# Optimization experiments

Hardware: AMD Instinct MI355X
Metric: run time of the kernel (lower is better)

## Reference

```python
import jax, jax.numpy as jnp
import numpy as np

B, L, C, H = 32, 512, 512, 8
DH = C // H
LN_EPS = 1e-5


def setup_inputs() -> dict:
    key = jax.random.key(0)
    ks = jax.random.split(key, 5)
    x = jax.random.normal(ks[0], (B, L, C), dtype=jnp.float32)
    # nn.Linear weights are (out, in); y = x @ W.T
    wq = jax.random.normal(ks[1], (C, C), dtype=jnp.float32) * 0.02
    wk = jax.random.normal(ks[2], (C, C), dtype=jnp.float32) * 0.02
    wv = jax.random.normal(ks[3], (C, C), dtype=jnp.float32) * 0.02
    # source zero-inits the bias table; use small randoms so it actually contributes
    bias_table = jax.random.normal(ks[4], (2 * L - 1, H), dtype=jnp.float32) * 0.02
    gamma = jnp.ones((C,), dtype=jnp.float32)
    beta = jnp.zeros((C,), dtype=jnp.float32)
    coords = np.arange(L)
    rel_index = jnp.asarray(coords[None, :] - coords[:, None] + (L - 1), dtype=jnp.int32)  # (L, L)
    return {"x": x, "wq": wq, "wk": wk, "wv": wv, "bias_table": bias_table,
            "gamma": gamma, "beta": beta, "rel_index": rel_index}


def reference(x, wq, wk, wv, bias_table, gamma, beta, rel_index):
    Bx, Lx, Cx = x.shape
    scale = Cx ** (-0.5)  # note: scale uses full emb_size, as in source
    q = (x @ wq.T).reshape(Bx, Lx, H, DH).transpose(0, 2, 1, 3)  # (B,H,L,Dh)
    k = (x @ wk.T).reshape(Bx, Lx, H, DH).transpose(0, 2, 1, 3)
    v = (x @ wv.T).reshape(Bx, Lx, H, DH).transpose(0, 2, 1, 3)
    attn = jax.nn.softmax(jnp.einsum('bhqd,bhkd->bhqk', q, k) * scale, axis=-1)
    # post-softmax relative bias gather-add
    rel_bias = bias_table[rel_index]                # (L, L, H)
    attn = attn + rel_bias.transpose(2, 0, 1)[None]  # (1,H,L,L) broadcast
    out = jnp.einsum('bhqk,bhkd->bhqd', attn, v)
    out = out.transpose(0, 2, 1, 3).reshape(Bx, Lx, Cx)
    mu = out.mean(axis=-1, keepdims=True)
    var = jnp.mean(jnp.square(out - mu), axis=-1, keepdims=True)
    return gamma * (out - mu) * jax.lax.rsqrt(var + LN_EPS) + beta
```

## Files before the change

kernel.cpp:

```cpp
#include <hip/hip_runtime.h>
#include <hip/hip_bf16.h>

typedef unsigned short u16;
typedef __attribute__((ext_vector_type(8))) __bf16 bf16x8;
typedef __attribute__((ext_vector_type(4))) float f32x4;
typedef __attribute__((ext_vector_type(4))) unsigned int u32x4;

#define BB 32
#define LL 512
#define CC 512
#define HH 8
#define DH 64
#define MROWS (BB * LL)
#define NQKV  (3 * CC)

#define XB_BYTES ((size_t)MROWS * CC * 2)
#define WC_BYTES ((size_t)NQKV * CC * 2)
#define QKV_OFF  (XB_BYTES + WC_BYTES)

#define SCALE2 (0.044194173824159216f * 1.4426950408889634f)

__device__ inline u16 f2b(float f) {
  union { float f; unsigned u; } a; a.f = f;
  unsigned u = a.u;
  return (u16)((u + 0x7FFFu + ((u >> 16) & 1u)) >> 16);
}

__device__ inline unsigned pack2(float a, float b) {
  float2 f; f.x = a; f.y = b;
  union { __hip_bfloat162 h; unsigned u; } c;
  c.h = __float22bfloat162_rn(f);
  return c.u;
}

__device__ inline bf16x8 gload16(const u16* p) {
  u32x4 r;
  asm volatile("global_load_dwordx4 %0, %1, off" : "=v"(r) : "v"(p));
  return __builtin_bit_cast(bf16x8, r);
}

__global__ __launch_bounds__(256) void cvt_x(const float* __restrict__ x, u16* __restrict__ xb) {
  int i = blockIdx.x * 256 + threadIdx.x;
  float4 v = ((const float4*)x)[i];
  uint2 o; o.x = pack2(v.x, v.y); o.y = pack2(v.z, v.w);
  ((uint2*)xb)[i] = o;
}

__global__ __launch_bounds__(256) void cvt_w(const float* __restrict__ wq, const float* __restrict__ wk,
                                             const float* __restrict__ wv, u16* __restrict__ wcat) {
  int i = blockIdx.x * 256 + threadIdx.x;
  int e = i * 4;
  int n = e >> 9;
  int k = e & 511;
  const float* src = (n < 512) ? (wq + (size_t)n * 512)
                   : (n < 1024) ? (wk + (size_t)(n - 512) * 512)
                                : (wv + (size_t)(n - 1024) * 512);
  const float sc = (n < 512) ? SCALE2 : 1.0f;
  float4 v = *(const float4*)(src + k);
  uint2 o; o.x = pack2(v.x * sc, v.y * sc); o.y = pack2(v.z * sc, v.w * sc);
  *(uint2*)(wcat + (size_t)n * 512 + k) = o;
}

__global__ __launch_bounds__(256) void bias_trans(const float* __restrict__ bias_table,
                                                  float* __restrict__ biasT) {
  int i = blockIdx.x * 256 + threadIdx.x;
  if (i < 1023 * 8) {
    float v = bias_table[i];
    int rel = i >> 3, hh = i & 7;
    biasT[hh * 1024 + rel] = v;
  }
}

typedef __attribute__((address_space(1))) void* as1_void_p;
typedef __attribute__((address_space(3))) void* as3_void_p;

__device__ inline void async16(const u16* g, u16* l) {
#if __has_builtin(__builtin_amdgcn_global_load_lds)
  __builtin_amdgcn_global_load_lds((as1_void_p)g, (as3_void_p)l, 16, 0, 0);
#else
  *(uint4*)l = *(const uint4*)g;
#endif
}

__global__ __launch_bounds__(256) void gemm_qkv(const u16* __restrict__ A, const u16* __restrict__ Bw,
                                                u16* __restrict__ Cm) {
  __shared__ u16 a_lds[128 * 32];
  __shared__ u16 b_lds[128 * 32];
  const int n0 = blockIdx.x * 128, m0 = blockIdx.y * 128;
  const int t = threadIdx.x, l = t & 63;
  const int wrow = ((t >> 7) & 1) * 64, wcol = ((t >> 6) & 1) * 64;
  const int lr = l & 15, lq = l >> 4;

  f32x4 acc[4][4] = {};

  for (int k0 = 0; k0 < 512; k0 += 32) {
    {
      int c0 = t, c1 = t + 256;
      async16(A  + (size_t)(m0 + (c0 >> 2)) * 512 + k0 + (c0 & 3) * 8, &a_lds[c0 * 8]);
      async16(A  + (size_t)(m0 + (c1 >> 2)) * 512 + k0 + (c1 & 3) * 8, &a_lds[c1 * 8]);
      async16(Bw + (size_t)(n0 + (c0 >> 2)) * 512 + k0 + (c0 & 3) * 8, &b_lds[c0 * 8]);
      async16(Bw + (size_t)(n0 + (c1 >> 2)) * 512 + k0 + (c1 & 3) * 8, &b_lds[c1 * 8]);
    }
    __syncthreads();
    bf16x8 af[4], bfr[4];
#pragma unroll
    for (int r = 0; r < 4; ++r) af[r]  = *(const bf16x8*)&a_lds[(wrow + r * 16 + lr) * 32 + lq * 8];
#pragma unroll
    for (int c = 0; c < 4; ++c) bfr[c] = *(const bf16x8*)&b_lds[(wcol + c * 16 + lr) * 32 + lq * 8];
#pragma unroll
    for (int r = 0; r < 4; ++r)
#pragma unroll
      for (int c = 0; c < 4; ++c)
        acc[r][c] = __builtin_amdgcn_mfma_f32_16x16x32_bf16(af[r], bfr[c], acc[r][c], 0, 0, 0);
    __syncthreads();
  }
#pragma unroll
  for (int r = 0; r < 4; ++r) {
#pragma unroll
    for (int i = 0; i < 4; ++i) {
      int m = m0 + wrow + r * 16 + lq * 4 + i;
      u16* crow = Cm + (size_t)m * NQKV + n0 + wcol;
#pragma unroll
      for (int c = 0; c < 4; ++c)
        crow[c * 16 + lr] = f2b(acc[r][c][i]);
    }
  }
}

__global__ __launch_bounds__(256) void transpose_v(const u16* __restrict__ qkv, u16* __restrict__ vT) {
  const int bh = blockIdx.x;
  const int b = bh >> 3, h = bh & 7;
  const int lc0 = blockIdx.y * 128;
  __shared__ u16 tile[32 * 72];
  const int t = threadIdx.x;
  for (int lc = lc0; lc < lc0 + 128; lc += 32) {
    int lrow = t >> 3, dcol = (t & 7) * 8;
    const u16* src = qkv + (size_t)(b * 512 + lc + lrow) * NQKV + 1024 + h * 64 + dcol;
    *(uint4*)&tile[lrow * 72 + dcol] = *(const uint4*)src;
    __syncthreads();
    int d = t >> 2, lp = (t & 3) * 8;
    union { ushort4 v4[2]; u16 s[8]; } tmp;
#pragma unroll
    for (int j = 0; j < 8; ++j) tmp.s[j] = tile[(lp + j) * 72 + d];
    *(uint4*)&vT[(size_t)(bh * 64 + d) * 512 + lc + lp] = *(uint4*)&tmp;
    __syncthreads();
  }
}

__global__ __launch_bounds__(256, 4) void attn_kernel(const u16* __restrict__ qkv, const u16* __restrict__ vT,
                                                      const float* __restrict__ biasT,
                                                      float* __restrict__ out) {
  __shared__ u16 p_lds[32 * 512];
  __shared__ float bias_lds[544];
  __shared__ float reds[4][32];

  const int flat = blockIdx.x;
  const int bh = ((flat >> 7) << 3) | (flat & 7);
  const int q0 = ((flat >> 3) & 15) * 32;
  const int b = bh >> 3, h = bh & 7;
  const int t = threadIdx.x, l = t & 63, w = t >> 6;
  const int lr = l & 15, lq = l >> 4;

  {
    const int rel0 = 480 - q0;
    const float* bsrc = biasT + h * 1024 + rel0;
    for (int i = t; i < 543; i += 256)
      bias_lds[i] = bsrc[i];
  }

  bf16x8 bq[2][2];
#pragma unroll
  for (int qt = 0; qt < 2; ++qt) {
    const u16* qrow = qkv + (size_t)(b * 512 + q0 + qt * 16 + lr) * NQKV + h * 64;
    bq[qt][0] = *(const bf16x8*)(qrow + lq * 8);
    bq[qt][1] = *(const bf16x8*)(qrow + 32 + lq * 8);
  }

  const u16* kbase = qkv + (size_t)(b * 512 + w * 128 + lr) * NQKV + 512 + h * 64 + lq * 8;
  bf16x8 ak[8][2];
#pragma unroll
  for (int ct = 0; ct < 8; ++ct) {
    const u16* kr = kbase + (size_t)ct * 16 * NQKV;
    ak[ct][0] = gload16(kr);
    ak[ct][1] = gload16(kr + 32);
  }
  asm volatile("s_waitcnt vmcnt(0)" ::: "memory");
  __builtin_amdgcn_sched_barrier(0);

  f32x4 sT[2][8];
#pragma unroll
  for (int ct = 0; ct < 8; ++ct) {
    f32x4 a0 = {0.f, 0.f, 0.f, 0.f}, a1 = {0.f, 0.f, 0.f, 0.f};
    a0 = __builtin_amdgcn_mfma_f32_16x16x32_bf16(ak[ct][0], bq[0][0], a0, 0, 0, 0);
    a0 = __builtin_amdgcn_mfma_f32_16x16x32_bf16(ak[ct][1], bq[0][1], a0, 0, 0, 0);
    a1 = __builtin_amdgcn_mfma_f32_16x16x32_bf16(ak[ct][0], bq[1][0], a1, 0, 0, 0);
    a1 = __builtin_amdgcn_mfma_f32_16x16x32_bf16(ak[ct][1], bq[1][1], a1, 0, 0, 0);
    sT[0][ct] = a0;
    sT[1][ct] = a1;
  }

  float sloc[2];
#pragma unroll
  for (int qt = 0; qt < 2; ++qt) {
    float s0 = 0.f, s1 = 0.f, s2 = 0.f, s3 = 0.f;
#pragma unroll
    for (int ct = 0; ct < 8; ++ct) {
      float e0 = exp2f(sT[qt][ct][0]);
      float e1 = exp2f(sT[qt][ct][1]);
      float e2 = exp2f(sT[qt][ct][2]);
      float e3 = exp2f(sT[qt][ct][3]);
      sT[qt][ct][0] = e0; sT[qt][ct][1] = e1;
      sT[qt][ct][2] = e2; sT[qt][ct][3] = e3;
      s0 += e0; s1 += e1; s2 += e2; s3 += e3;
    }
    float s = (s0 + s1) + (s2 + s3);
    s += __shfl_xor(s, 16, 64);
    s += __shfl_xor(s, 32, 64);
    sloc[qt] = s;
  }
  if (lq == 0) { reds[w][lr] = sloc[0]; reds[w][16 + lr] = sloc[1]; }
  __syncthreads();
  float rinv[2];
#pragma unroll
  for (int qt = 0; qt < 2; ++qt)
    rinv[qt] = 1.0f / (reds[0][qt * 16 + lr] + reds[1][qt * 16 + lr] +
                       reds[2][qt * 16 + lr] + reds[3][qt * 16 + lr]);

  const u16* vrow = vT + (size_t)(bh * 64 + w * 16 + lr) * 512 + lq * 8;
  bf16x8 av[16];
#pragma unroll
  for (int kb = 0; kb < 8; ++kb) av[kb] = gload16(vrow + kb * 32);

#define PACK_QT(qt)                                                            \
  {                                                                            \
    const int qlocal = (qt) * 16 + lr;                                         \
    u16* prow = p_lds + qlocal * 512;                                          \
    const int boff = w * 128 + lq * 4 + 31 - qlocal;                           \
    _Pragma("unroll")                                                          \
    for (int ct = 0; ct < 8; ++ct) {                                           \
      const int gsw = w * 8 + (ct ^ (lr & 7));                                 \
      float p0 = sT[qt][ct][0] * rinv[qt] + bias_lds[boff + ct * 16 + 0];      \
      float p1 = sT[qt][ct][1] * rinv[qt] + bias_lds[boff + ct * 16 + 1];      \
      float p2 = sT[qt][ct][2] * rinv[qt] + bias_lds[boff + ct * 16 + 2];      \
      float p3 = sT[qt][ct][3] * rinv[qt] + bias_lds[boff + ct * 16 + 3];      \
      uint2 pk; pk.x = pack2(p0, p1); pk.y = pack2(p2, p3);                    \
      *(uint2*)&prow[gsw * 16 + lq * 4] = pk;                                  \
    }                                                                          \
  }

  PACK_QT(0)
#pragma unroll
  for (int kb = 8; kb < 16; ++kb) av[kb] = gload16(vrow + kb * 32);
  PACK_QT(1)
#undef PACK_QT

  __syncthreads();
  asm volatile("s_waitcnt vmcnt(0)" ::: "memory");
  __builtin_amdgcn_sched_barrier(0);

  f32x4 accP[2] = {};
  bf16x8 bp[4][2];
#define LDP(kb, qt) \
  (*(const bf16x8*)&p_lds[((qt) * 16 + lr) * 512 + \
    (((2 * (kb) + (lq >> 1)) & ~7) | (((2 * (kb) + (lq >> 1)) & 7) ^ (lr & 7))) * 16 + (lq & 1) * 8])
#pragma unroll
  for (int pre = 0; pre < 3; ++pre) { bp[pre][0] = LDP(pre, 0); bp[pre][1] = LDP(pre, 1); }
#pragma unroll
  for (int kb = 0; kb < 16; ++kb) {
    if (kb < 13) {
      bp[(kb + 3) & 3][0] = LDP(kb + 3, 0);
      bp[(kb + 3) & 3][1] = LDP(kb + 3, 1);
    }
    accP[0] = __builtin_amdgcn_mfma_f32_16x16x32_bf16(av[kb], bp[kb & 3][0], accP[0], 0, 0, 0);
    accP[1] = __builtin_amdgcn_mfma_f32_16x16x32_bf16(av[kb], bp[kb & 3][1], accP[1], 0, 0, 0);
  }
#undef LDP
#pragma unroll
  for (int qt = 0; qt < 2; ++qt)
    *(f32x4*)&out[(size_t)(b * 512 + q0 + qt * 16 + lr) * 512 + h * 64 + w * 16 + lq * 4] = accP[qt];
}

__global__ __launch_bounds__(256) void ln_kernel(float* __restrict__ out,
                                                 const float* __restrict__ gamma,
                                                 const float* __restrict__ beta) {
  const int t = threadIdx.x;
  const int r2 = t >> 7;
  const int row = blockIdx.x * 2 + r2;
  const int c = (t & 127) * 4;
  float* p = out + (size_t)row * 512;
  float4 v = *(float4*)(p + c);
  float s = v.x + v.y + v.z + v.w;
  float s2 = v.x * v.x + v.y * v.y + v.z * v.z + v.w * v.w;
#pragma unroll
  for (int d = 1; d < 64; d <<= 1) { s += __shfl_xor(s, d, 64); s2 += __shfl_xor(s2, d, 64); }
  __shared__ float ps[4], ps2[4];
  const int wv = t >> 6;
  if ((t & 63) == 0) { ps[wv] = s; ps2[wv] = s2; }
  __syncthreads();
  s  = ps[r2 * 2]  + ps[r2 * 2 + 1];
  s2 = ps2[r2 * 2] + ps2[r2 * 2 + 1];
  float mu = s * (1.0f / 512.0f);
  float var = s2 * (1.0f / 512.0f) - mu * mu;
  float rs = rsqrtf(var + 1e-5f);
  float4 g = *(const float4*)(gamma + c);
  float4 bb = *(const float4*)(beta + c);
  v.x = g.x * (v.x - mu) * rs + bb.x;
  v.y = g.y * (v.y - mu) * rs + bb.y;
  v.z = g.z * (v.z - mu) * rs + bb.z;
  v.w = g.w * (v.w - mu) * rs + bb.w;
  *(float4*)(p + c) = v;
}

extern "C" void kernel_launch(void* const* d_in, const int* in_sizes, int n_in,
                              void* d_out, int out_size, void* d_ws, size_t ws_size,
                              hipStream_t stream) {
  const float* x    = (const float*)d_in[0];
  const float* wq   = (const float*)d_in[1];
  const float* wk   = (const float*)d_in[2];
  const float* wv   = (const float*)d_in[3];
  const float* bias = (const float*)d_in[4];
  const float* gamma = (const float*)d_in[5];
  const float* beta  = (const float*)d_in[6];
  float* out = (float*)d_out;

  char* ws = (char*)d_ws;
  u16* xb   = (u16*)ws;
  u16* wcat = (u16*)(ws + XB_BYTES);
  u16* qkv  = (u16*)(ws + QKV_OFF);
  u16* vT   = xb;
  float* biasT = (float*)(ws + XB_BYTES);

  cvt_x<<<dim3((MROWS * CC) / 4 / 256), 256, 0, stream>>>(x, xb);
  cvt_w<<<dim3((NQKV * CC) / 4 / 256), 256, 0, stream>>>(wq, wk, wv, wcat);
  gemm_qkv<<<dim3(NQKV / 128, MROWS / 128), 256, 0, stream>>>(xb, wcat, qkv);
  bias_trans<<<dim3(32), 256, 0, stream>>>(bias, biasT);
  transpose_v<<<dim3(256, 4), 256, 0, stream>>>(qkv, vT);
  attn_kernel<<<dim3(16 * 256), 256, 0, stream>>>(qkv, vT, biasT, out);
  ln_kernel<<<dim3(MROWS / 2), 256, 0, stream>>>(out, gamma, beta);
}
```

Before: 227.8 us.

## Fold bias transpose into transpose_v, pair global loads, add MFMA priority hints

The separate bias_trans launch is merged into transpose_v as an extra grid row, which removes one kernel launch. In attn_kernel, K and V global loads are issued in pairs through inline asm using immediate offsets, which saves address arithmetic. The MFMA sections are wrapped in s_setprio raise and lower hints, and the occupancy hint in launch_bounds drops from 4 to 3 blocks per CU. The lower occupancy hint gives the compiler more registers but may reduce latency hiding.

```diff
diff --git a/kernel.cpp b/kernel.cpp
--- a/kernel.cpp
+++ b/kernel.cpp
@@ -31,12 +31,6 @@
   union { __hip_bfloat162 h; unsigned u; } c;
   c.h = __float22bfloat162_rn(f);
   return c.u;
-}
-
-__device__ inline bf16x8 gload16(const u16* p) {
-  u32x4 r;
-  asm volatile("global_load_dwordx4 %0, %1, off" : "=v"(r) : "v"(p));
-  return __builtin_bit_cast(bf16x8, r);
 }
 
 __global__ __launch_bounds__(256) void cvt_x(const float* __restrict__ x, u16* __restrict__ xb) {
@@ -61,16 +55,6 @@
   *(uint2*)(wcat + (size_t)n * 512 + k) = o;
 }
 
-__global__ __launch_bounds__(256) void bias_trans(const float* __restrict__ bias_table,
-                                                  float* __restrict__ biasT) {
-  int i = blockIdx.x * 256 + threadIdx.x;
-  if (i < 1023 * 8) {
-    float v = bias_table[i];
-    int rel = i >> 3, hh = i & 7;
-    biasT[hh * 1024 + rel] = v;
-  }
-}
-
 typedef __attribute__((address_space(1))) void* as1_void_p;
 typedef __attribute__((address_space(3))) void* as3_void_p;
 
@@ -127,7 +111,20 @@
   }
 }
 
-__global__ __launch_bounds__(256) void transpose_v(const u16* __restrict__ qkv, u16* __restrict__ vT) {
+__global__ __launch_bounds__(256) void transpose_v(const u16* __restrict__ qkv, u16* __restrict__ vT,
+                                                   const float* __restrict__ bias_table,
+                                                   float* __restrict__ biasT) {
+  if (blockIdx.y == 4) {
+    if (blockIdx.x < 32) {
+      int i = blockIdx.x * 256 + threadIdx.x;
+      if (i < 1023 * 8) {
+        float v = bias_table[i];
+        int rel = i >> 3, hh = i & 7;
+        biasT[hh * 1024 + rel] = v;
+      }
+    }
+    return;
+  }
   const int bh = blockIdx.x;
   const int b = bh >> 3, h = bh & 7;
   const int lc0 = blockIdx.y * 128;
@@ -147,7 +144,7 @@
   }
 }
 
-__global__ __launch_bounds__(256, 4) void attn_kernel(const u16* __restrict__ qkv, const u16* __restrict__ vT,
+__global__ __launch_bounds__(256, 3) void attn_kernel(const u16* __restrict__ qkv, const u16* __restrict__ vT,
                                                       const float* __restrict__ biasT,
                                                       float* __restrict__ out) {
   __shared__ u16 p_lds[32 * 512];
@@ -177,29 +174,34 @@
   }
 
   const u16* kbase = qkv + (size_t)(b * 512 + w * 128 + lr) * NQKV + 512 + h * 64 + lq * 8;
-  bf16x8 ak[8][2];
+  u32x4 akr[8][2];
 #pragma unroll
   for (int ct = 0; ct < 8; ++ct) {
     const u16* kr = kbase + (size_t)ct * 16 * NQKV;
-    ak[ct][0] = gload16(kr);
-    ak[ct][1] = gload16(kr + 32);
+    asm volatile("global_load_dwordx4 %0, %2, off\n\t"
+                 "global_load_dwordx4 %1, %2, off offset:64"
+                 : "=&v"(akr[ct][0]), "=&v"(akr[ct][1]) : "v"(kr));
   }
   asm volatile("s_waitcnt vmcnt(0)" ::: "memory");
   __builtin_amdgcn_sched_barrier(0);
 
   f32x4 sT[2][8];
+  __builtin_amdgcn_s_setprio(1);
 #pragma unroll
   for (int ct = 0; ct < 8; ++ct) {
+    bf16x8 ak0 = __builtin_bit_cast(bf16x8, akr[ct][0]);
+    bf16x8 ak1 = __builtin_bit_cast(bf16x8, akr[ct][1]);
     f32x4 a0 = {0.f, 0.f, 0.f, 0.f}, a1 = {0.f, 0.f, 0.f, 0.f};
-    a0 = __builtin_amdgcn_mfma_f32_16x16x32_bf16(ak[ct][0], bq[0][0], a0, 0, 0, 0);
-    a0 = __builtin_amdgcn_mfma_f32_16x16x32_bf16(ak[ct][1], bq[0][1], a0, 0, 0, 0);
-    a1 = __builtin_amdgcn_mfma_f32_16x16x32_bf16(ak[ct][0], bq[1][0], a1, 0, 0, 0);
-    a1 = __builtin_amdgcn_mfma_f32_16x16x32_bf16(ak[ct][1], bq[1][1], a1, 0, 0, 0);
+    a0 = __builtin_amdgcn_mfma_f32_16x16x32_bf16(ak0, bq[0][0], a0, 0, 0, 0);
+    a0 = __builtin_amdgcn_mfma_f32_16x16x32_bf16(ak1, bq[0][1], a0, 0, 0, 0);
+    a1 = __builtin_amdgcn_mfma_f32_16x16x32_bf16(ak0, bq[1][0], a1, 0, 0, 0);
+    a1 = __builtin_amdgcn_mfma_f32_16x16x32_bf16(ak1, bq[1][1], a1, 0, 0, 0);
     sT[0][ct] = a0;
     sT[1][ct] = a1;
   }
-
-  float sloc[2];
+  __builtin_amdgcn_s_setprio(0);
+
+  float sq[2];
 #pragma unroll
   for (int qt = 0; qt < 2; ++qt) {
     float s0 = 0.f, s1 = 0.f, s2 = 0.f, s3 = 0.f;
@@ -213,12 +215,16 @@
       sT[qt][ct][2] = e2; sT[qt][ct][3] = e3;
       s0 += e0; s1 += e1; s2 += e2; s3 += e3;
     }
-    float s = (s0 + s1) + (s2 + s3);
-    s += __shfl_xor(s, 16, 64);
-    s += __shfl_xor(s, 32, 64);
-    sloc[qt] = s;
-  }
-  if (lq == 0) { reds[w][lr] = sloc[0]; reds[w][16 + lr] = sloc[1]; }
+    sq[qt] = (s0 + s1) + (s2 + s3);
+  }
+  {
+    float t0 = sq[0], t1 = sq[1];
+    float u0 = __shfl_xor(t0, 16, 64), u1 = __shfl_xor(t1, 16, 64);
+    t0 += u0; t1 += u1;
+    u0 = __shfl_xor(t0, 32, 64); u1 = __shfl_xor(t1, 32, 64);
+    sq[0] = t0 + u0; sq[1] = t1 + u1;
+  }
+  if (lq == 0) { reds[w][lr] = sq[0]; reds[w][16 + lr] = sq[1]; }
   __syncthreads();
   float rinv[2];
 #pragma unroll
@@ -227,9 +233,12 @@
                        reds[2][qt * 16 + lr] + reds[3][qt * 16 + lr]);
 
   const u16* vrow = vT + (size_t)(bh * 64 + w * 16 + lr) * 512 + lq * 8;
-  bf16x8 av[16];
-#pragma unroll
-  for (int kb = 0; kb < 8; ++kb) av[kb] = gload16(vrow + kb * 32);
+  u32x4 avr[16];
+#define GLV(i, o0, o1)                                                         \
+  asm volatile("global_load_dwordx4 %0, %2, off offset:" o0 "\n\t"             \
+               "global_load_dwordx4 %1, %2, off offset:" o1                    \
+               : "=&v"(avr[i]), "=&v"(avr[(i) + 1]) : "v"(vrow))
+  GLV(0, "0", "64"); GLV(2, "128", "192"); GLV(4, "256", "320"); GLV(6, "384", "448");
 
 #define PACK_QT(qt)                                                            \
   {                                                                            \
@@ -249,8 +258,8 @@
   }
 
   PACK_QT(0)
-#pragma unroll
-  for (int kb = 8; kb < 16; ++kb) av[kb] = gload16(vrow + kb * 32);
+  GLV(8, "512", "576"); GLV(10, "640", "704"); GLV(12, "768", "832"); GLV(14, "896", "960");
+#undef GLV
   PACK_QT(1)
 #undef PACK_QT
 
@@ -265,15 +274,18 @@
     (((2 * (kb) + (lq >> 1)) & ~7) | (((2 * (kb) + (lq >> 1)) & 7) ^ (lr & 7))) * 16 + (lq & 1) * 8])
 #pragma unroll
   for (int pre = 0; pre < 3; ++pre) { bp[pre][0] = LDP(pre, 0); bp[pre][1] = LDP(pre, 1); }
+  __builtin_amdgcn_s_setprio(1);
 #pragma unroll
   for (int kb = 0; kb < 16; ++kb) {
     if (kb < 13) {
       bp[(kb + 3) & 3][0] = LDP(kb + 3, 0);
       bp[(kb + 3) & 3][1] = LDP(kb + 3, 1);
     }
-    accP[0] = __builtin_amdgcn_mfma_f32_16x16x32_bf16(av[kb], bp[kb & 3][0], accP[0], 0, 0, 0);
-    accP[1] = __builtin_amdgcn_mfma_f32_16x16x32_bf16(av[kb], bp[kb & 3][1], accP[1], 0, 0, 0);
-  }
+    bf16x8 av = __builtin_bit_cast(bf16x8, avr[kb]);
+    accP[0] = __builtin_amdgcn_mfma_f32_16x16x32_bf16(av, bp[kb & 3][0], accP[0], 0, 0, 0);
+    accP[1] = __builtin_amdgcn_mfma_f32_16x16x32_bf16(av, bp[kb & 3][1], accP[1], 0, 0, 0);
+  }
+  __builtin_amdgcn_s_setprio(0);
 #undef LDP
 #pragma unroll
   for (int qt = 0; qt < 2; ++qt)
@@ -333,8 +345,7 @@
   cvt_x<<<dim3((MROWS * CC) / 4 / 256), 256, 0, stream>>>(x, xb);
   cvt_w<<<dim3((NQKV * CC) / 4 / 256), 256, 0, stream>>>(wq, wk, wv, wcat);
   gemm_qkv<<<dim3(NQKV / 128, MROWS / 128), 256, 0, stream>>>(xb, wcat, qkv);
-  bias_trans<<<dim3(32), 256, 0, stream>>>(bias, biasT);
-  transpose_v<<<dim3(256, 4), 256, 0, stream>>>(qkv, vT);
+  transpose_v<<<dim3(256, 5), 256, 0, stream>>>(qkv, vT, bias, biasT);
   attn_kernel<<<dim3(16 * 256), 256, 0, stream>>>(qkv, vT, biasT, out);
   ln_kernel<<<dim3(MROWS / 2), 256, 0, stream>>>(out, gamma, beta);
 }
```

Result: no change. 227.0 us (-0.3%).
